# Optimization experiments

Measured on AMD Instinct MI355X. Metric: run time of the kernel, lower is better.

Reference implementation:

```python
import jax, jax.numpy as jnp
import numpy as np

B, S, HID = 4, 128, 4096
D, HQ, HK = 128, 32, 8
PAGES, PSIZE, NPP = 64, 256, 16  # page pool, page size, pages per sequence
THETA = 10000.0
EPS = 1e-6
SCALE = 1.0 / float(np.sqrt(D))


def setup_inputs() -> dict:
    key = jax.random.key(0)
    ks = jax.random.split(key, 10)
    x = jax.random.normal(ks[0], (B, S, HID), jnp.float32)
    Wq = jax.random.normal(ks[1], (HQ * D, HID), jnp.float32) * 0.02
    Wk = jax.random.normal(ks[2], (HK * D, HID), jnp.float32) * 0.02
    Wv = jax.random.normal(ks[3], (HK * D, HID), jnp.float32) * 0.02
    Wo = jax.random.normal(ks[4], (HID, HQ * D), jnp.float32) * 0.02
    q_norm_w = jax.random.uniform(ks[5], (D,), jnp.float32)
    k_norm_w = jax.random.uniform(ks[6], (D,), jnp.float32)
    k_cache = jax.random.normal(ks[7], (PAGES, PSIZE, HK, D), jnp.float32)
    v_cache = jax.random.normal(ks[8], (PAGES, PSIZE, HK, D), jnp.float32)
    block_table = jnp.arange(B * NPP, dtype=jnp.int32).reshape(B, NPP)
    cache_seqlens = jax.random.randint(ks[9], (B,), 0, 3800).astype(jnp.int32)
    return dict(x=x, Wq=Wq, Wk=Wk, Wv=Wv, Wo=Wo, q_norm_w=q_norm_w,
                k_norm_w=k_norm_w, k_cache=k_cache, v_cache=v_cache,
                block_table=block_table, cache_seqlens=cache_seqlens)


def _rmsnorm(t, w):
    # per-head RMSNorm over head_dim (constant_bias = 0)
    var = jnp.mean(t * t, axis=-1, keepdims=True)
    return t * jax.lax.rsqrt(var + EPS) * w


def _rope(t, pos):
    # NeoX-style half-rotation. t: [B,S,H,D], pos: [B,S]
    inv_freq = 1.0 / (THETA ** (jnp.arange(0, D, 2, dtype=jnp.float32) / D))  # [D/2]
    freqs = pos[..., None].astype(jnp.float32) * inv_freq                     # [B,S,D/2]
    cos = jnp.cos(freqs)[:, :, None, :]
    sin = jnp.sin(freqs)[:, :, None, :]
    t1, t2 = t[..., : D // 2], t[..., D // 2:]
    return jnp.concatenate([t1 * cos - t2 * sin, t2 * cos + t1 * sin], axis=-1)


def reference(x, Wq, Wk, Wv, Wo, q_norm_w, k_norm_w, k_cache, v_cache,
              block_table, cache_seqlens):
    bsz, seqlen, _ = x.shape
    # QKV projections
    q = jnp.einsum('bsd,ed->bse', x, Wq).reshape(bsz, seqlen, HQ, D)
    k = jnp.einsum('bsd,ed->bse', x, Wk).reshape(bsz, seqlen, HK, D)
    v = jnp.einsum('bsd,ed->bse', x, Wv).reshape(bsz, seqlen, HK, D)
    # QK-norm then RoPE (fused norm+rope path of the module)
    q = _rmsnorm(q, q_norm_w)
    k = _rmsnorm(k, k_norm_w)
    pos = cache_seqlens[:, None] + jnp.arange(seqlen)[None, :]  # [B,S]
    q = _rope(q, pos)
    k = _rope(k, pos)
    # Gather paged KV cache: [B, NPP*PSIZE, HK, D]
    L = NPP * PSIZE
    kc = k_cache[block_table].reshape(bsz, L, HK, D)
    vc = v_cache[block_table].reshape(bsz, L, HK, D)
    # Append new tokens (flash_attn_with_kvcache writes k,v into the cache)
    k_all = jnp.concatenate([kc, k], axis=1)  # [B, L+S, HK, D]
    v_all = jnp.concatenate([vc, v], axis=1)
    # Valid mask: cache slots < cache_seqlens; all new keys valid (causal=False, full window)
    valid_c = jnp.arange(L)[None, :] < cache_seqlens[:, None]          # [B, L]
    valid = jnp.concatenate(
        [valid_c, jnp.ones((bsz, seqlen), dtype=bool)], axis=1)        # [B, L+S]
    rep = HQ // HK
    k_all = jnp.repeat(k_all, rep, axis=2)
    v_all = jnp.repeat(v_all, rep, axis=2)
    scores = jnp.einsum('bqhd,bkhd->bhqk', q, k_all) * SCALE
    scores = jnp.where(valid[:, None, None, :], scores, -1e30)
    probs = jax.nn.softmax(scores, axis=-1)
    o = jnp.einsum('bhqk,bkhd->bqhd', probs, v_all)
    o = o.reshape(bsz, seqlen, HQ * D)
    return jnp.einsum('bse,de->bsd', o, Wo)
```

## Files before the change

### kernel.cpp

```cpp
#include <hip/hip_runtime.h>

typedef unsigned short u16;
typedef float f4v __attribute__((ext_vector_type(4)));
typedef short s8v __attribute__((ext_vector_type(8)));
typedef int   i4v __attribute__((ext_vector_type(4)));

#define SCALE_ 0.08838834764831845f

__device__ __forceinline__ u16 f2b(float f) {
    union { float f; unsigned u; } c; c.f = f;
    unsigned u = c.u + 0x7fffu + ((c.u >> 16) & 1u);
    return (u16)(u >> 16);
}

typedef const __attribute__((address_space(1))) unsigned int gu32;
typedef __attribute__((address_space(3))) unsigned int lu32;
__device__ __forceinline__ void glds16(const void* g, void* l) {
    __builtin_amdgcn_global_load_lds((gu32*)g, (lu32*)l, 16, 0, 0);
}

template <int ABF16>
__global__ __launch_bounds__(256) void fgemm_sk(const void* __restrict__ Ap,
                                                const float* __restrict__ Bp,
                                                float* __restrict__ Cp,
                                                int M, int N, int K, int Ksl) {
    __shared__ __align__(16) char At[64 * 128];
    __shared__ __align__(16) char Bt[128 * 128];
    const int tid = threadIdx.x, lane = tid & 63, wid = tid >> 6;
    const int lm = lane & 15, lg = lane >> 4;
    const int m0 = blockIdx.y * 64, n0 = blockIdx.x * 128;
    const int k0 = blockIdx.z * Ksl;
    const int NT = Ksl >> 6;
    Cp += (size_t)blockIdx.z * M * N;

    f4v acc[4][2];
#pragma unroll
    for (int mi = 0; mi < 4; mi++)
#pragma unroll
        for (int ni = 0; ni < 2; ni++) acc[mi][ni] = (f4v){0.f, 0.f, 0.f, 0.f};

    float fA[2][8];
    s8v   hA[2];
    float fB[4][8];

    auto loadT = [&](int kt) {
#pragma unroll
        for (int i = 0; i < 2; i++) {
            int c = tid + i * 256; int r = c >> 3, k8 = c & 7;
            if constexpr (ABF16) {
                hA[i] = *(const s8v*)((const u16*)Ap + (size_t)(m0 + r) * K + k0 + kt * 64 + k8 * 8);
            } else {
                const float* p = (const float*)Ap + (size_t)(m0 + r) * K + k0 + kt * 64 + k8 * 8;
                float4 u = *(const float4*)p, v = *(const float4*)(p + 4);
                fA[i][0] = u.x; fA[i][1] = u.y; fA[i][2] = u.z; fA[i][3] = u.w;
                fA[i][4] = v.x; fA[i][5] = v.y; fA[i][6] = v.z; fA[i][7] = v.w;
            }
        }
#pragma unroll
        for (int i = 0; i < 4; i++) {
            int c = tid + i * 256; int r = c >> 3, k8 = c & 7;
            const float* p = Bp + (size_t)(n0 + r) * K + k0 + kt * 64 + k8 * 8;
            float4 u = *(const float4*)p, v = *(const float4*)(p + 4);
            fB[i][0] = u.x; fB[i][1] = u.y; fB[i][2] = u.z; fB[i][3] = u.w;
            fB[i][4] = v.x; fB[i][5] = v.y; fB[i][6] = v.z; fB[i][7] = v.w;
        }
    };

    auto storeLDS = [&]() {
#pragma unroll
        for (int i = 0; i < 2; i++) {
            int c = tid + i * 256; int r = c >> 3, k8 = c & 7;
            s8v hv;
            if constexpr (ABF16) hv = hA[i];
            else {
#pragma unroll
                for (int j = 0; j < 8; j++) hv[j] = (short)f2b(fA[i][j]);
            }
            *(s8v*)(At + ((r * 128 + k8 * 16) ^ ((r & 7) << 4))) = hv;
        }
#pragma unroll
        for (int i = 0; i < 4; i++) {
            int c = tid + i * 256; int r = c >> 3, k8 = c & 7;
            s8v hv;
#pragma unroll
            for (int j = 0; j < 8; j++) hv[j] = (short)f2b(fB[i][j]);
            *(s8v*)(Bt + ((r * 128 + k8 * 16) ^ ((r & 7) << 4))) = hv;
        }
    };

    loadT(0);
    for (int kt = 0; kt < NT; ++kt) {
        __syncthreads();
        storeLDS();
        __syncthreads();
        if (kt + 1 < NT) loadT(kt + 1);
#pragma unroll
        for (int ks = 0; ks < 2; ks++) {
            s8v av[4], bv[2];
#pragma unroll
            for (int mi = 0; mi < 4; mi++) {
                int r = mi * 16 + lm;
                av[mi] = *(const s8v*)(At + ((r * 128 + ks * 64 + lg * 16) ^ ((r & 7) << 4)));
            }
#pragma unroll
            for (int ni = 0; ni < 2; ni++) {
                int r = wid * 32 + ni * 16 + lm;
                bv[ni] = *(const s8v*)(Bt + ((r * 128 + ks * 64 + lg * 16) ^ ((r & 7) << 4)));
            }
#pragma unroll
            for (int mi = 0; mi < 4; mi++)
#pragma unroll
                for (int ni = 0; ni < 2; ni++)
                    acc[mi][ni] = __builtin_amdgcn_mfma_f32_16x16x32_bf16(av[mi], bv[ni], acc[mi][ni], 0, 0, 0);
        }
    }

#pragma unroll
    for (int mi = 0; mi < 4; mi++)
#pragma unroll
        for (int ni = 0; ni < 2; ni++)
#pragma unroll
            for (int r = 0; r < 4; r++) {
                int m = m0 + mi * 16 + lg * 4 + r;
                int n = n0 + wid * 32 + ni * 16 + lm;
                Cp[(size_t)m * N + n] = acc[mi][ni][r];
            }
}

__global__ __launch_bounds__(256) void nrope_k(const float* __restrict__ src,
                                               u16* __restrict__ dst,
                                               const float* __restrict__ w,
                                               const int* __restrict__ cseq,
                                               int nheads, float oscale,
                                               int nsl, size_t sls) {
    const int lane = threadIdx.x & 63;
    const int rid = blockIdx.x * 4 + (threadIdx.x >> 6);
    const int s = (rid / nheads) & 127;
    const int b = rid / (nheads * 128);
    const float* p = src + (size_t)rid * 128;
    float x1 = 0.f, x2 = 0.f;
    for (int sl = 0; sl < nsl; sl++) {
        x1 += p[sl * sls + lane];
        x2 += p[sl * sls + lane + 64];
    }
    float ss = x1 * x1 + x2 * x2;
#pragma unroll
    for (int off = 1; off < 64; off <<= 1) ss += __shfl_xor(ss, off);
    float inv = rsqrtf(ss * (1.0f / 128.0f) + 1e-6f);
    float n1 = x1 * inv * w[lane];
    float n2 = x2 * inv * w[lane + 64];
    float pos = (float)(cseq[b] + s);
    float ang = pos * powf(10000.0f, -(float)lane * (1.0f / 64.0f));
    float cs = cosf(ang), sn = sinf(ang);
    dst[(size_t)rid * 128 + lane]      = f2b((n1 * cs - n2 * sn) * oscale);
    dst[(size_t)rid * 128 + lane + 64] = f2b((n2 * cs + n1 * sn) * oscale);
}

__global__ __launch_bounds__(256) void cvt_bf16k(const float* __restrict__ s,
                                                 u16* __restrict__ d, int n4,
                                                 int nsl, size_t sls) {
    int i = blockIdx.x * blockDim.x + threadIdx.x;
    if (i < n4) {
        f4v f = (f4v){0.f, 0.f, 0.f, 0.f};
        for (int sl = 0; sl < nsl; sl++)
            f += *(const f4v*)(s + sl * sls + (size_t)i * 4);
        ushort4 o;
        o.x = f2b(f[0]); o.y = f2b(f[1]); o.z = f2b(f[2]); o.w = f2b(f[3]);
        ((ushort4*)d)[i] = o;
    }
}

__global__ __launch_bounds__(256) void red4_k(const float* __restrict__ p,
                                              float* __restrict__ out, int n4,
                                              size_t sls) {
    int i = blockIdx.x * blockDim.x + threadIdx.x;
    if (i < n4) {
        f4v s = (f4v){0.f, 0.f, 0.f, 0.f};
#pragma unroll
        for (int sl = 0; sl < 4; sl++)
            s += *(const f4v*)(p + sl * sls + (size_t)i * 4);
        *(f4v*)(out + (size_t)i * 4) = s;
    }
}

__global__ __launch_bounds__(256) void cvtkv_k(const float* __restrict__ kc,
                                               const float* __restrict__ vc,
                                               const u16* __restrict__ kb,
                                               const u16* __restrict__ vb,
                                               const int* __restrict__ btab,
                                               const int* __restrict__ cseq,
                                               u16* __restrict__ kb2,
                                               u16* __restrict__ vb2) {
    const int t = blockIdx.x, hk = blockIdx.y, b = blockIdx.z;
    const int tid = threadIdx.x;
    const int cl = cseq[b];
    if (t < 64 && t * 64 >= cl) return;
    u16* kout = kb2 + ((size_t)(b * 8 + hk) * 66 + t) * 8192;
    u16* vout = vb2 + ((size_t)(b * 8 + hk) * 66 + t) * 8192;

    if (t < 64) {
#pragma unroll
        for (int i = 0; i < 4; i++) {
            int c = tid + i * 256; int r = c >> 4, c16 = c & 15;
            int cc = c16 ^ (r & 7);
            int p = t * 64 + r;
            const float* src = kc + (((size_t)btab[b * 16 + (p >> 8)] * 256 + (p & 255)) * 8 + hk) * 128 + cc * 8;
            float4 f0 = *(const float4*)src, f1 = *(const float4*)(src + 4);
            s8v v;
            v[0] = (short)f2b(f0.x); v[1] = (short)f2b(f0.y); v[2] = (short)f2b(f0.z); v[3] = (short)f2b(f0.w);
            v[4] = (short)f2b(f1.x); v[5] = (short)f2b(f1.y); v[6] = (short)f2b(f1.z); v[7] = (short)f2b(f1.w);
            *(s8v*)(kout + r * 128 + c16 * 8) = v;
        }
#pragma unroll
        for (int i = 0; i < 4; i++) {
            int c = tid + i * 256; int pr = c >> 5, c16v = c & 31;
            int nc = c16v ^ pr;
            int n = nc * 4;
            int p = t * 64 + pr * 2;
            const float* s0 = vc + (((size_t)btab[b * 16 + (p >> 8)] * 256 + (p & 255)) * 8 + hk) * 128 + n;
            float4 e = *(const float4*)s0, o = *(const float4*)(s0 + 1024);
            i4v w;
            w[0] = (int)((unsigned)f2b(e.x) | ((unsigned)f2b(o.x) << 16));
            w[1] = (int)((unsigned)f2b(e.y) | ((unsigned)f2b(o.y) << 16));
            w[2] = (int)((unsigned)f2b(e.z) | ((unsigned)f2b(o.z) << 16));
            w[3] = (int)((unsigned)f2b(e.w) | ((unsigned)f2b(o.w) << 16));
            *(i4v*)(vout + pr * 256 + c16v * 8) = w;
        }
    } else {
        int s0r = (t - 64) * 64;
#pragma unroll
        for (int i = 0; i < 4; i++) {
            int c = tid + i * 256; int r = c >> 4, c16 = c & 15;
            int cc = c16 ^ (r & 7);
            s8v v = *(const s8v*)(kb + ((size_t)(b * 128 + s0r + r) * 8 + hk) * 128 + cc * 8);
            *(s8v*)(kout + r * 128 + c16 * 8) = v;
        }
#pragma unroll
        for (int i = 0; i < 4; i++) {
            int c = tid + i * 256; int pr = c >> 5, c16v = c & 31;
            int nc = c16v ^ pr;
            int n = nc * 4;
            const u16* s0 = vb + ((size_t)(b * 128 + s0r + pr * 2) * 8 + hk) * 128 + n;
            ushort4 e = *(const ushort4*)s0, o = *(const ushort4*)(s0 + 1024);
            i4v w;
            w[0] = (int)((unsigned)e.x | ((unsigned)o.x << 16));
            w[1] = (int)((unsigned)e.y | ((unsigned)o.y << 16));
            w[2] = (int)((unsigned)e.z | ((unsigned)o.z << 16));
            w[3] = (int)((unsigned)e.w | ((unsigned)o.w << 16));
            *(i4v*)(vout + pr * 256 + c16v * 8) = w;
        }
    }
}

__global__ __launch_bounds__(256) void fattn2_k(const u16* __restrict__ qb,
                                                const u16* __restrict__ kb2,
                                                const u16* __restrict__ vb2,
                                                const int* __restrict__ cseq,
                                                float* __restrict__ po,
                                                float* __restrict__ mb,
                                                float* __restrict__ lb) {
    __shared__ __align__(16) char Ks[2][16384];
    __shared__ __align__(16) char Vs[2][16384];
    __shared__ __align__(16) char Ps[4][2048];

    const int tid = threadIdx.x, lane = tid & 63, wid = tid >> 6;
    const int lm = lane & 15, lg = lane >> 4;
    const int bid = blockIdx.x;
    const int sp = bid & 3, half = (bid >> 2) & 1, h = (bid >> 3) & 31, b = bid >> 8;
    const int hk = h >> 2;

    s8v qa[4];
    {
        const u16* qp = qb + ((size_t)((b * 128 + half * 64 + wid * 16 + lm) * 32 + h)) * 128 + lg * 8;
#pragma unroll
        for (int ks = 0; ks < 4; ks++) qa[ks] = *(const s8v*)(qp + ks * 32);
    }

    float m_run[4], l_run[4];
    f4v acc[8];
#pragma unroll
    for (int r = 0; r < 4; r++) { m_run[r] = -1e30f; l_run[r] = 0.f; }
#pragma unroll
    for (int dt = 0; dt < 8; dt++) acc[dt] = (f4v){0.f, 0.f, 0.f, 0.f};

    const int cl = cseq[b];
    const int ntc = (cl + 63) >> 6;
    const int tlo = (ntc * sp) >> 2, thi = (ntc * (sp + 1)) >> 2;
    const int ncache = thi - tlo;
    const int ntiles = ncache + (sp == 3 ? 2 : 0);

    const char* gk = (const char*)kb2 + (size_t)(b * 8 + hk) * 66 * 16384;
    const char* gv = (const char*)vb2 + (size_t)(b * 8 + hk) * 66 * 16384;

    auto STAGE = [&](int buf, int gt) {
        const char* gkt = gk + (size_t)gt * 16384 + wid * 4096 + lane * 16;
        const char* gvt = gv + (size_t)gt * 16384 + wid * 4096 + lane * 16;
        char* lk = Ks[buf] + wid * 4096;
        char* lv = Vs[buf] + wid * 4096;
#pragma unroll
        for (int i = 0; i < 4; i++) {
            glds16(gkt + i * 1024, lk + i * 1024);
            glds16(gvt + i * 1024, lv + i * 1024);
        }
    };
    auto GT = [&](int ii) { return ii < ncache ? tlo + ii : 64 + (ii - ncache); };

    if (ntiles > 0) STAGE(0, GT(0));
    asm volatile("s_waitcnt vmcnt(0)" ::: "memory");
    __syncthreads();

    for (int ii = 0; ii < ntiles; ++ii) {
        const int cur = ii & 1;
        if (ii + 1 < ntiles) STAGE(cur ^ 1, GT(ii + 1));
        const int gt = GT(ii);
        const int t0 = gt * 64;

        f4v sc[4];
#pragma unroll
        for (int ct = 0; ct < 4; ct++) sc[ct] = (f4v){0.f, 0.f, 0.f, 0.f};
#pragma unroll
        for (int ct = 0; ct < 4; ct++) {
#pragma unroll
            for (int ks = 0; ks < 4; ks++) {
                int r = ct * 16 + lm;
                s8v kf = *(const s8v*)(Ks[cur] + ((r * 256 + ks * 64 + lg * 16) ^ ((r & 7) << 4)));
                sc[ct] = __builtin_amdgcn_mfma_f32_16x16x32_bf16(qa[ks], kf, sc[ct], 0, 0, 0);
            }
        }
        if (gt < 64 && (t0 + 64 > cl)) {
#pragma unroll
            for (int ct = 0; ct < 4; ct++) {
                int p = t0 + ct * 16 + lm;
                if (p >= cl) { sc[ct][0] = -1e30f; sc[ct][1] = -1e30f; sc[ct][2] = -1e30f; sc[ct][3] = -1e30f; }
            }
        }

        float mnew[4], corr[4], rsum[4];
#pragma unroll
        for (int r = 0; r < 4; r++) {
            float mt = fmaxf(fmaxf(sc[0][r], sc[1][r]), fmaxf(sc[2][r], sc[3][r]));
#pragma unroll
            for (int off = 1; off < 16; off <<= 1) mt = fmaxf(mt, __shfl_xor(mt, off));
            float mn = fmaxf(m_run[r], mt);
            corr[r] = __expf(m_run[r] - mn);
            m_run[r] = mn;
            mnew[r] = mn;
            rsum[r] = 0.f;
        }
#pragma unroll
        for (int ct = 0; ct < 4; ct++) {
#pragma unroll
            for (int r = 0; r < 4; r++) {
                float pv = __expf(sc[ct][r] - mnew[r]);
                rsum[r] += pv;
                int row = lg * 4 + r;
                *(u16*)(Ps[wid] + ((row * 128 + (ct * 16 + lm) * 2) ^ ((row & 7) << 4))) = f2b(pv);
            }
        }
#pragma unroll
        for (int r = 0; r < 4; r++) {
            float rs = rsum[r];
#pragma unroll
            for (int off = 1; off < 16; off <<= 1) rs += __shfl_xor(rs, off);
            l_run[r] = l_run[r] * corr[r] + rs;
        }
#pragma unroll
        for (int dt = 0; dt < 8; dt++) {
#pragma unroll
            for (int r = 0; r < 4; r++) acc[dt][r] *= corr[r];
        }

        s8v pa[2];
#pragma unroll
        for (int k2 = 0; k2 < 2; k2++)
            pa[k2] = *(const s8v*)(Ps[wid] + ((lm * 128 + k2 * 64 + lg * 16) ^ ((lm & 7) << 4)));

#pragma unroll
        for (int k2 = 0; k2 < 2; k2++) {
#pragma unroll
            for (int dt = 0; dt < 8; dt++) {
                i4v vv;
#pragma unroll
                for (int t = 0; t < 4; t++) {
                    int p = k2 * 16 + lg * 4 + t;
                    vv[t] = *(const int*)(Vs[cur] + p * 512 + ((((dt * 16 + lm) * 4)) ^ ((p & 31) << 4)));
                }
                union { i4v i; s8v s; } u; u.i = vv;
                acc[dt] = __builtin_amdgcn_mfma_f32_16x16x32_bf16(pa[k2], u.s, acc[dt], 0, 0, 0);
            }
        }

        asm volatile("s_waitcnt vmcnt(0)" ::: "memory");
        __syncthreads();
    }

#pragma unroll
    for (int dt = 0; dt < 8; dt++) {
#pragma unroll
        for (int r = 0; r < 4; r++) {
            int row = wid * 16 + lg * 4 + r;
            po[((size_t)bid * 64 + row) * 128 + dt * 16 + lm] = acc[dt][r];
        }
    }
    if (lm == 0) {
#pragma unroll
        for (int r = 0; r < 4; r++) {
            int row = wid * 16 + lg * 4 + r;
            mb[(size_t)bid * 64 + row] = m_run[r];
            lb[(size_t)bid * 64 + row] = l_run[r];
        }
    }
}

__global__ __launch_bounds__(256) void fcomb_k(const float* __restrict__ po,
                                               const float* __restrict__ mb,
                                               const float* __restrict__ lb,
                                               u16* __restrict__ ob) {
    const int pid = blockIdx.x, t = threadIdx.x;
    const int row = t >> 2, dq = t & 3;
    const int half = pid & 1, h = (pid >> 1) & 31, b = pid >> 6;
    float m[4], l[4];
#pragma unroll
    for (int i = 0; i < 4; i++) {
        m[i] = mb[(size_t)(pid * 4 + i) * 64 + row];
        l[i] = lb[(size_t)(pid * 4 + i) * 64 + row];
    }
    float M = fmaxf(fmaxf(m[0], m[1]), fmaxf(m[2], m[3]));
    float w[4], L = 0.f;
#pragma unroll
    for (int i = 0; i < 4; i++) { w[i] = __expf(m[i] - M); L += w[i] * l[i]; }
    float invL = 1.0f / L;
    u16* dst = ob + ((size_t)(b * 128 + half * 64 + row) * 32 + h) * 128 + dq * 32;
#pragma unroll
    for (int j = 0; j < 8; j++) {
        f4v s = (f4v){0.f, 0.f, 0.f, 0.f};
#pragma unroll
        for (int i = 0; i < 4; i++) {
            f4v a = *(const f4v*)(po + ((size_t)(pid * 4 + i) * 64 + row) * 128 + dq * 32 + j * 4);
            s += w[i] * a;
        }
        ushort4 o;
        o.x = f2b(s[0] * invL); o.y = f2b(s[1] * invL);
        o.z = f2b(s[2] * invL); o.w = f2b(s[3] * invL);
        *(ushort4*)(dst + j * 4) = o;
    }
}

extern "C" void kernel_launch(void* const* d_in, const int* in_sizes, int n_in,
                              void* d_out, int out_size, void* d_ws, size_t ws_size,
                              hipStream_t stream) {
    const float* x   = (const float*)d_in[0];
    const float* Wq  = (const float*)d_in[1];
    const float* Wk  = (const float*)d_in[2];
    const float* Wv  = (const float*)d_in[3];
    const float* Wo  = (const float*)d_in[4];
    const float* qnw = (const float*)d_in[5];
    const float* knw = (const float*)d_in[6];
    const float* kc  = (const float*)d_in[7];
    const float* vc  = (const float*)d_in[8];
    const int* btab  = (const int*)d_in[9];
    const int* cseq  = (const int*)d_in[10];
    float* out = (float*)d_out;

    char* ws = (char*)d_ws;
    u16*   qb   = (u16*)(ws + 0);
    u16*   kb   = (u16*)(ws + 4194304);
    u16*   vb   = (u16*)(ws + 5242880);
    u16*   ob   = (u16*)(ws + 6291456);
    float* mbuf = (float*)(ws + 10485760);
    float* lbuf = (float*)(ws + 10747904);
    float* pA   = (float*)(ws + 11010048);
    float* po   = (float*)(ws + 11010048);
    u16*   kb2  = (u16*)(ws + 44564480);
    u16*   vb2  = (u16*)(ws + 79167488);
    float* pK   = (float*)(ws + 79167488);
    float* pV   = (float*)(ws + 95944704);

    dim3 blk(256, 1, 1);
    fgemm_sk<0><<<dim3(32, 8, 4), blk, 0, stream>>>(x, Wq, pA, 512, 4096, 4096, 1024);
    fgemm_sk<0><<<dim3(8, 8, 8),  blk, 0, stream>>>(x, Wk, pK, 512, 1024, 4096, 512);
    fgemm_sk<0><<<dim3(8, 8, 8),  blk, 0, stream>>>(x, Wv, pV, 512, 1024, 4096, 512);
    nrope_k<<<dim3(4096, 1, 1), blk, 0, stream>>>(pA, qb, qnw, cseq, 32, SCALE_, 4, (size_t)512 * 4096);
    nrope_k<<<dim3(1024, 1, 1), blk, 0, stream>>>(pK, kb, knw, cseq, 8, 1.0f, 8, (size_t)512 * 1024);
    cvt_bf16k<<<dim3(512, 1, 1), blk, 0, stream>>>(pV, vb, 131072, 8, (size_t)512 * 1024);
    cvtkv_k<<<dim3(66, 8, 4), blk, 0, stream>>>(kc, vc, kb, vb, btab, cseq, kb2, vb2);
    fattn2_k<<<dim3(1024, 1, 1), blk, 0, stream>>>(qb, kb2, vb2, cseq, po, mbuf, lbuf);
    fcomb_k<<<dim3(256, 1, 1), blk, 0, stream>>>(po, mbuf, lbuf, ob);
    fgemm_sk<1><<<dim3(32, 8, 4), blk, 0, stream>>>(ob, Wo, pA, 512, 4096, 4096, 1024);
    red4_k<<<dim3(2048, 1, 1), blk, 0, stream>>>(pA, out, 2097152, (size_t)512 * 4096);
}
```

Baseline: 265.5 us.

## Pre-convert GEMM operands to tiled swizzled bf16 and stage via async LDS loads

Result: no change. 270.0 us (+1.7%).

```diff
diff --git a/kernel.cpp b/kernel.cpp
--- a/kernel.cpp
+++ b/kernel.cpp
@@ -19,18 +19,39 @@
     __builtin_amdgcn_global_load_lds((gu32*)g, (lu32*)l, 16, 0, 0);
 }
 
-template <int ABF16>
-__global__ __launch_bounds__(256) void fgemm_sk(const void* __restrict__ Ap,
-                                                const float* __restrict__ Bp,
-                                                float* __restrict__ Cp,
-                                                int M, int N, int K, int Ksl) {
-    __shared__ __align__(16) char At[64 * 128];
-    __shared__ __align__(16) char Bt[128 * 128];
+template <int RB>
+__global__ __launch_bounds__(256) void wcvt_k(const float* __restrict__ src,
+                                              u16* __restrict__ dst, int K) {
+    const int kt = blockIdx.x, nt = blockIdx.y;
+    u16* out = dst + ((size_t)nt * gridDim.x + kt) * (RB * 64);
+#pragma unroll
+    for (int i = 0; i < RB / 32; i++) {
+        int c = threadIdx.x + i * 256;
+        int r = c >> 3, c16 = c & 7, cc = c16 ^ (r & 7);
+        const float* p = src + (size_t)(nt * RB + r) * K + kt * 64 + cc * 8;
+        float4 f0 = *(const float4*)p, f1 = *(const float4*)(p + 4);
+        s8v v;
+        v[0] = (short)f2b(f0.x); v[1] = (short)f2b(f0.y);
+        v[2] = (short)f2b(f0.z); v[3] = (short)f2b(f0.w);
+        v[4] = (short)f2b(f1.x); v[5] = (short)f2b(f1.y);
+        v[6] = (short)f2b(f1.z); v[7] = (short)f2b(f1.w);
+        *(s8v*)(out + r * 64 + c16 * 8) = v;
+    }
+}
+
+__global__ __launch_bounds__(256) void fgemm2(const u16* __restrict__ Ag,
+                                              const u16* __restrict__ Bg,
+                                              float* __restrict__ Cp,
+                                              int M, int N, int K, int Ksl) {
+    __shared__ __align__(16) u16 As[2][4096];
+    __shared__ __align__(16) u16 Bs[2][8192];
     const int tid = threadIdx.x, lane = tid & 63, wid = tid >> 6;
     const int lm = lane & 15, lg = lane >> 4;
     const int m0 = blockIdx.y * 64, n0 = blockIdx.x * 128;
-    const int k0 = blockIdx.z * Ksl;
-    const int NT = Ksl >> 6;
+    const int KT = K >> 6, NT = Ksl >> 6;
+    const int kt0 = (blockIdx.z * Ksl) >> 6;
+    const u16* ga = Ag + ((size_t)blockIdx.y * KT + kt0) * 4096;
+    const u16* gb = Bg + ((size_t)blockIdx.x * KT + kt0) * 8192;
     Cp += (size_t)blockIdx.z * M * N;
 
     f4v acc[4][2];
@@ -39,73 +60,36 @@
 #pragma unroll
         for (int ni = 0; ni < 2; ni++) acc[mi][ni] = (f4v){0.f, 0.f, 0.f, 0.f};
 
-    float fA[2][8];
-    s8v   hA[2];
-    float fB[4][8];
-
-    auto loadT = [&](int kt) {
-#pragma unroll
-        for (int i = 0; i < 2; i++) {
-            int c = tid + i * 256; int r = c >> 3, k8 = c & 7;
-            if constexpr (ABF16) {
-                hA[i] = *(const s8v*)((const u16*)Ap + (size_t)(m0 + r) * K + k0 + kt * 64 + k8 * 8);
-            } else {
-                const float* p = (const float*)Ap + (size_t)(m0 + r) * K + k0 + kt * 64 + k8 * 8;
-                float4 u = *(const float4*)p, v = *(const float4*)(p + 4);
-                fA[i][0] = u.x; fA[i][1] = u.y; fA[i][2] = u.z; fA[i][3] = u.w;
-                fA[i][4] = v.x; fA[i][5] = v.y; fA[i][6] = v.z; fA[i][7] = v.w;
-            }
-        }
-#pragma unroll
-        for (int i = 0; i < 4; i++) {
-            int c = tid + i * 256; int r = c >> 3, k8 = c & 7;
-            const float* p = Bp + (size_t)(n0 + r) * K + k0 + kt * 64 + k8 * 8;
-            float4 u = *(const float4*)p, v = *(const float4*)(p + 4);
-            fB[i][0] = u.x; fB[i][1] = u.y; fB[i][2] = u.z; fB[i][3] = u.w;
-            fB[i][4] = v.x; fB[i][5] = v.y; fB[i][6] = v.z; fB[i][7] = v.w;
-        }
+    auto STAGE = [&](int buf, int kt) {
+        const char* a = (const char*)(ga + (size_t)kt * 4096) + tid * 16;
+        const char* b = (const char*)(gb + (size_t)kt * 8192) + tid * 16;
+        char* la = (char*)As[buf] + tid * 16;
+        char* lb = (char*)Bs[buf] + tid * 16;
+        glds16(a, la);
+        glds16(a + 4096, la + 4096);
+#pragma unroll
+        for (int i = 0; i < 4; i++) glds16(b + i * 4096, lb + i * 4096);
     };
 
-    auto storeLDS = [&]() {
-#pragma unroll
-        for (int i = 0; i < 2; i++) {
-            int c = tid + i * 256; int r = c >> 3, k8 = c & 7;
-            s8v hv;
-            if constexpr (ABF16) hv = hA[i];
-            else {
-#pragma unroll
-                for (int j = 0; j < 8; j++) hv[j] = (short)f2b(fA[i][j]);
-            }
-            *(s8v*)(At + ((r * 128 + k8 * 16) ^ ((r & 7) << 4))) = hv;
-        }
-#pragma unroll
-        for (int i = 0; i < 4; i++) {
-            int c = tid + i * 256; int r = c >> 3, k8 = c & 7;
-            s8v hv;
-#pragma unroll
-            for (int j = 0; j < 8; j++) hv[j] = (short)f2b(fB[i][j]);
-            *(s8v*)(Bt + ((r * 128 + k8 * 16) ^ ((r & 7) << 4))) = hv;
-        }
-    };
-
-    loadT(0);
+    STAGE(0, 0);
+    asm volatile("s_waitcnt vmcnt(0)" ::: "memory");
+    __syncthreads();
+
     for (int kt = 0; kt < NT; ++kt) {
-        __syncthreads();
-        storeLDS();
-        __syncthreads();
-        if (kt + 1 < NT) loadT(kt + 1);
+        const int cur = kt & 1;
+        if (kt + 1 < NT) STAGE(cur ^ 1, kt + 1);
 #pragma unroll
         for (int ks = 0; ks < 2; ks++) {
             s8v av[4], bv[2];
 #pragma unroll
             for (int mi = 0; mi < 4; mi++) {
                 int r = mi * 16 + lm;
-                av[mi] = *(const s8v*)(At + ((r * 128 + ks * 64 + lg * 16) ^ ((r & 7) << 4)));
+                av[mi] = *(const s8v*)(As[cur] + r * 64 + (((ks * 4 + lg) ^ (r & 7)) * 8));
             }
 #pragma unroll
             for (int ni = 0; ni < 2; ni++) {
                 int r = wid * 32 + ni * 16 + lm;
-                bv[ni] = *(const s8v*)(Bt + ((r * 128 + ks * 64 + lg * 16) ^ ((r & 7) << 4)));
+                bv[ni] = *(const s8v*)(Bs[cur] + r * 64 + (((ks * 4 + lg) ^ (r & 7)) * 8));
             }
 #pragma unroll
             for (int mi = 0; mi < 4; mi++)
@@ -113,6 +97,8 @@
                 for (int ni = 0; ni < 2; ni++)
                     acc[mi][ni] = __builtin_amdgcn_mfma_f32_16x16x32_bf16(av[mi], bv[ni], acc[mi][ni], 0, 0, 0);
         }
+        asm volatile("s_waitcnt vmcnt(0)" ::: "memory");
+        __syncthreads();
     }
 
 #pragma unroll
@@ -415,7 +401,7 @@
 __global__ __launch_bounds__(256) void fcomb_k(const float* __restrict__ po,
                                                const float* __restrict__ mb,
                                                const float* __restrict__ lb,
-                                               u16* __restrict__ ob) {
+                                               u16* __restrict__ obT) {
     const int pid = blockIdx.x, t = threadIdx.x;
     const int row = t >> 2, dq = t & 3;
     const int half = pid & 1, h = (pid >> 1) & 31, b = pid >> 6;
@@ -430,7 +416,8 @@
 #pragma unroll
     for (int i = 0; i < 4; i++) { w[i] = __expf(m[i] - M); L += w[i] * l[i]; }
     float invL = 1.0f / L;
-    u16* dst = ob + ((size_t)(b * 128 + half * 64 + row) * 32 + h) * 128 + dq * 32;
+    const int arow = b * 128 + half * 64 + row;
+    const int mt = arow >> 6, rr = arow & 63;
 #pragma unroll
     for (int j = 0; j < 8; j++) {
         f4v s = (f4v){0.f, 0.f, 0.f, 0.f};
@@ -442,7 +429,9 @@
         ushort4 o;
         o.x = f2b(s[0] * invL); o.y = f2b(s[1] * invL);
         o.z = f2b(s[2] * invL); o.w = f2b(s[3] * invL);
-        *(ushort4*)(dst + j * 4) = o;
+        const int acol = h * 128 + dq * 32 + j * 4;
+        const int kt = acol >> 6, cch = (acol >> 3) & 7, wo = acol & 7;
+        *(ushort4*)(obT + ((size_t)(mt * 64 + kt)) * 4096 + rr * 64 + ((cch ^ (rr & 7)) * 8) + wo) = o;
     }
 }
 
@@ -466,26 +455,37 @@
     u16*   qb   = (u16*)(ws + 0);
     u16*   kb   = (u16*)(ws + 4194304);
     u16*   vb   = (u16*)(ws + 5242880);
-    u16*   ob   = (u16*)(ws + 6291456);
+    u16*   obT  = (u16*)(ws + 6291456);
+    u16*   xb   = (u16*)(ws + 6291456);
     float* mbuf = (float*)(ws + 10485760);
     float* lbuf = (float*)(ws + 10747904);
-    float* pA   = (float*)(ws + 11010048);
-    float* po   = (float*)(ws + 11010048);
+    float* P    = (float*)(ws + 11010048);
+    u16*   wW   = (u16*)(ws + 44564480);
     u16*   kb2  = (u16*)(ws + 44564480);
     u16*   vb2  = (u16*)(ws + 79167488);
-    float* pK   = (float*)(ws + 79167488);
-    float* pV   = (float*)(ws + 95944704);
 
     dim3 blk(256, 1, 1);
-    fgemm_sk<0><<<dim3(32, 8, 4), blk, 0, stream>>>(x, Wq, pA, 512, 4096, 4096, 1024);
-    fgemm_sk<0><<<dim3(8, 8, 8),  blk, 0, stream>>>(x, Wk, pK, 512, 1024, 4096, 512);
-    fgemm_sk<0><<<dim3(8, 8, 8),  blk, 0, stream>>>(x, Wv, pV, 512, 1024, 4096, 512);
-    nrope_k<<<dim3(4096, 1, 1), blk, 0, stream>>>(pA, qb, qnw, cseq, 32, SCALE_, 4, (size_t)512 * 4096);
-    nrope_k<<<dim3(1024, 1, 1), blk, 0, stream>>>(pK, kb, knw, cseq, 8, 1.0f, 8, (size_t)512 * 1024);
-    cvt_bf16k<<<dim3(512, 1, 1), blk, 0, stream>>>(pV, vb, 131072, 8, (size_t)512 * 1024);
+    const size_t slsQ = (size_t)512 * 4096, slsKV = (size_t)512 * 1024;
+
+    wcvt_k<64><<<dim3(64, 8, 1), blk, 0, stream>>>(x, xb, 4096);
+
+    wcvt_k<128><<<dim3(64, 32, 1), blk, 0, stream>>>(Wq, wW, 4096);
+    fgemm2<<<dim3(32, 8, 4), blk, 0, stream>>>(xb, wW, P, 512, 4096, 4096, 1024);
+    nrope_k<<<dim3(4096, 1, 1), blk, 0, stream>>>(P, qb, qnw, cseq, 32, SCALE_, 4, slsQ);
+
+    wcvt_k<128><<<dim3(64, 8, 1), blk, 0, stream>>>(Wk, wW, 4096);
+    fgemm2<<<dim3(8, 8, 8), blk, 0, stream>>>(xb, wW, P, 512, 1024, 4096, 512);
+    nrope_k<<<dim3(1024, 1, 1), blk, 0, stream>>>(P, kb, knw, cseq, 8, 1.0f, 8, slsKV);
+
+    wcvt_k<128><<<dim3(64, 8, 1), blk, 0, stream>>>(Wv, wW, 4096);
+    fgemm2<<<dim3(8, 8, 8), blk, 0, stream>>>(xb, wW, P, 512, 1024, 4096, 512);
+    cvt_bf16k<<<dim3(512, 1, 1), blk, 0, stream>>>(P, vb, 131072, 8, slsKV);
+
     cvtkv_k<<<dim3(66, 8, 4), blk, 0, stream>>>(kc, vc, kb, vb, btab, cseq, kb2, vb2);
-    fattn2_k<<<dim3(1024, 1, 1), blk, 0, stream>>>(qb, kb2, vb2, cseq, po, mbuf, lbuf);
-    fcomb_k<<<dim3(256, 1, 1), blk, 0, stream>>>(po, mbuf, lbuf, ob);
-    fgemm_sk<1><<<dim3(32, 8, 4), blk, 0, stream>>>(ob, Wo, pA, 512, 4096, 4096, 1024);
-    red4_k<<<dim3(2048, 1, 1), blk, 0, stream>>>(pA, out, 2097152, (size_t)512 * 4096);
-}
+    fattn2_k<<<dim3(1024, 1, 1), blk, 0, stream>>>(qb, kb2, vb2, cseq, P, mbuf, lbuf);
+    fcomb_k<<<dim3(256, 1, 1), blk, 0, stream>>>(P, mbuf, lbuf, obT);
+
+    wcvt_k<128><<<dim3(64, 32, 1), blk, 0, stream>>>(Wo, wW, 4096);
+    fgemm2<<<dim3(32, 8, 4), blk, 0, stream>>>(obT, wW, P, 512, 4096, 4096, 1024);
+    red4_k<<<dim3(2048, 1, 1), blk, 0, stream>>>(P, out, 2097152, slsQ);
+}
```
